# Kernel tuning notes

Measured on AMD Instinct MI355X. Metric: run time of the kernel, lower is better.

## Reference

```python
import jax, jax.numpy as jnp
import numpy as np

N_NODES = 50000
N_EDGES = 800000
D_IN = 128
D_OUT = 128


def setup_inputs() -> dict:
    key = jax.random.key(0)
    k1, k2, k3, k4 = jax.random.split(key, 4)
    feature = jax.random.normal(k1, (N_NODES, D_IN), dtype=jnp.float32)
    relation_indices = jax.random.randint(k2, (2, N_EDGES), 0, N_NODES, dtype=jnp.int64)
    relation_weight = jax.random.uniform(k3, (N_EDGES, 1), dtype=jnp.float32)
    W = jax.random.normal(k4, (2 * D_IN, D_OUT), dtype=jnp.float32) * (1.0 / np.sqrt(2 * D_IN))
    b = jnp.zeros((D_OUT,), dtype=jnp.float32)
    return {"feature": feature, "relation_indices": relation_indices,
            "relation_weight": relation_weight, "W": W, "b": b}


def reference(feature, relation_indices, relation_weight, W, b):
    dst = relation_indices[0]  # segment ids (aggregation target) [E]
    src = relation_indices[1]  # neighbor ids gathered from feature [E]
    # gather neighbor features and apply edge weights (dropout_rate=0 -> identity)
    feat_n = feature[src] * relation_weight  # [E, D_IN]
    # segment mean over destination nodes
    n = feature.shape[0]
    sums = jax.ops.segment_sum(feat_n, dst, num_segments=n)  # [N, D_IN]
    cnts = jax.ops.segment_sum(jnp.ones((feat_n.shape[0],), dtype=feat_n.dtype), dst, num_segments=n)
    neigh_mean = sums / jnp.maximum(cnts, 1.0)[:, None]
    # concat(self, mean_neighbor) -> linear update
    h = jnp.concatenate([feature, neigh_mean], axis=-1)  # [N, 2*D_IN]
    return h @ W + b  # [N, D_OUT]
```

## Files before the change

### kernel.cpp

```cpp
#include <hip/hip_runtime.h>
#include <hip/hip_bf16.h>
#include <stdint.h>

#define N_NODES 50000
#define N_EDGES 800000
#define D 128
#define NB_SCAN 196

typedef __attribute__((ext_vector_type(8))) short bf16x8;
typedef __attribute__((ext_vector_type(4))) float f32x4;
typedef __attribute__((ext_vector_type(2))) short bf16x2;

#define FEATBF_OFF 0
#define MEANBF_OFF 12800000
#define WSW_OFF    25600000
#define HIST_OFF   25665536
#define OFFS_OFF   25865536
#define CURS_OFF   26065552
#define EDGE_OFF   26265552
#define BSUM_OFF   29465552
#define BOFF_OFF   29466576

__device__ inline short f2bf(float x) {
  union { float f; uint32_t u; } v; v.f = x;
  uint32_t r = v.u + 0x7FFFu + ((v.u >> 16) & 1u);
  return (short)(r >> 16);
}
__device__ inline float bf2f(uint32_t bits16) {
  union { uint32_t u; float f; } v; v.u = bits16 << 16;
  return v.f;
}

__global__ __launch_bounds__(256) void k_prep(const float* __restrict__ feat,
                                              const int* __restrict__ idx,
                                              const float* __restrict__ W,
                                              short* __restrict__ featbf,
                                              int* __restrict__ hist,
                                              short* __restrict__ wsw) {
  int b = blockIdx.x;
  if (b < 3125) {
    int i = (b * 256 + threadIdx.x) * 8;
    f32x4 a0 = *(const f32x4*)(feat + i);
    f32x4 a1 = *(const f32x4*)(feat + i + 4);
    bf16x8 o;
    o[0] = f2bf(a0.x); o[1] = f2bf(a0.y); o[2] = f2bf(a0.z); o[3] = f2bf(a0.w);
    o[4] = f2bf(a1.x); o[5] = f2bf(a1.y); o[6] = f2bf(a1.z); o[7] = f2bf(a1.w);
    *(bf16x8*)(featbf + i) = o;
  } else if (b < 6250) {
    int e = (b - 3125) * 256 + threadIdx.x;
    atomicAdd(&hist[idx[e]], 1);
  } else {
    int t = (b - 6250) * 256 + threadIdx.x;
    int kstep = t >> 9;
    int ntile = (t >> 6) & 7;
    int lane  = t & 63;
    int k0  = kstep * 32 + (lane >> 4) * 8;
    int col = ntile * 16 + (lane & 15);
    bf16x8 o;
    #pragma unroll
    for (int j = 0; j < 8; ++j) o[j] = f2bf(W[(k0 + j) * D + col]);
    *(bf16x8*)(wsw + t * 8) = o;
  }
}

__global__ __launch_bounds__(256) void k_scan1(const int* __restrict__ hist,
                                               int* __restrict__ blockSum) {
  __shared__ int red[256];
  int t = threadIdx.x;
  int i = blockIdx.x * 256 + t;
  red[t] = (i < N_NODES) ? hist[i] : 0;
  __syncthreads();
  #pragma unroll
  for (int s = 128; s > 0; s >>= 1) {
    if (t < s) red[t] += red[t + s];
    __syncthreads();
  }
  if (t == 0) blockSum[blockIdx.x] = red[0];
}

__global__ __launch_bounds__(256) void k_scan2(const int* __restrict__ blockSum,
                                               int* __restrict__ blockOff,
                                               int* __restrict__ offs) {
  __shared__ int lds[256];
  int t = threadIdx.x;
  int v = (t < NB_SCAN) ? blockSum[t] : 0;
  lds[t] = v;
  __syncthreads();
  #pragma unroll
  for (int off = 1; off < 256; off <<= 1) {
    int add = (t >= off) ? lds[t - off] : 0;
    __syncthreads();
    lds[t] += add;
    __syncthreads();
  }
  if (t < NB_SCAN) blockOff[t] = lds[t] - v;
  if (t == 255) offs[N_NODES] = lds[255];
}

__global__ __launch_bounds__(256) void k_scan3(const int* __restrict__ hist,
                                               const int* __restrict__ blockOff,
                                               int* __restrict__ offs,
                                               int* __restrict__ cursor) {
  __shared__ int lds[256];
  int t = threadIdx.x;
  int i = blockIdx.x * 256 + t;
  int v = (i < N_NODES) ? hist[i] : 0;
  lds[t] = v;
  __syncthreads();
  #pragma unroll
  for (int off = 1; off < 256; off <<= 1) {
    int add = (t >= off) ? lds[t - off] : 0;
    __syncthreads();
    lds[t] += add;
    __syncthreads();
  }
  int excl = lds[t] - v + blockOff[blockIdx.x];
  if (i < N_NODES) { offs[i] = excl; cursor[i] = excl; }
}

__global__ __launch_bounds__(256) void k_scatter(const int* __restrict__ idx,
                                                 const float* __restrict__ w,
                                                 int* __restrict__ cursor,
                                                 uint32_t* __restrict__ edge) {
  int e = blockIdx.x * 256 + threadIdx.x;
  if (e < N_EDGES) {
    int dst = idx[e];
    int p = atomicAdd(&cursor[dst], 1);
    uint32_t src = (uint32_t)idx[N_EDGES + e];
    uint32_t wb  = (uint32_t)f2bf(w[e]) & 0xFFFFu;
    edge[p] = (src << 16) | wb;
  }
}

__global__ __launch_bounds__(256) void k_agg(const short* __restrict__ featbf,
                                             const int* __restrict__ offs,
                                             const uint32_t* __restrict__ edge,
                                             short* __restrict__ meanbf) {
  int t = blockIdx.x * 256 + threadIdx.x;
  int node = t >> 6;
  int c = t & 63;
  if (node >= N_NODES) return;
  int beg = offs[node], end = offs[node + 1];

  float a0 = 0.f, a1 = 0.f, b0 = 0.f, b1 = 0.f;
  float c0 = 0.f, c1 = 0.f, d0 = 0.f, d1 = 0.f;

  int j = beg;
  for (; j + 3 < end; j += 4) {
    uint32_t e0 = edge[j + 0];
    uint32_t e1 = edge[j + 1];
    uint32_t e2 = edge[j + 2];
    uint32_t e3 = edge[j + 3];
    bf16x2 f0 = *(const bf16x2*)(featbf + (size_t)(e0 >> 16) * D + c * 2);
    bf16x2 f1 = *(const bf16x2*)(featbf + (size_t)(e1 >> 16) * D + c * 2);
    bf16x2 f2 = *(const bf16x2*)(featbf + (size_t)(e2 >> 16) * D + c * 2);
    bf16x2 f3 = *(const bf16x2*)(featbf + (size_t)(e3 >> 16) * D + c * 2);
    float w0 = bf2f(e0 & 0xFFFFu), w1 = bf2f(e1 & 0xFFFFu);
    float w2 = bf2f(e2 & 0xFFFFu), w3 = bf2f(e3 & 0xFFFFu);
    a0 += bf2f((uint16_t)f0[0]) * w0;  a1 += bf2f((uint16_t)f0[1]) * w0;
    b0 += bf2f((uint16_t)f1[0]) * w1;  b1 += bf2f((uint16_t)f1[1]) * w1;
    c0 += bf2f((uint16_t)f2[0]) * w2;  c1 += bf2f((uint16_t)f2[1]) * w2;
    d0 += bf2f((uint16_t)f3[0]) * w3;  d1 += bf2f((uint16_t)f3[1]) * w3;
  }
  for (; j < end; ++j) {
    uint32_t ed = edge[j];
    float wt = bf2f(ed & 0xFFFFu);
    bf16x2 f = *(const bf16x2*)(featbf + (size_t)(ed >> 16) * D + c * 2);
    a0 += bf2f((uint16_t)f[0]) * wt;
    a1 += bf2f((uint16_t)f[1]) * wt;
  }
  float s0 = (a0 + b0) + (c0 + d0);
  float s1 = (a1 + b1) + (c1 + d1);

  float invc = 1.0f / fmaxf((float)(end - beg), 1.0f);
  bf16x2 o;
  o[0] = f2bf(s0 * invc);
  o[1] = f2bf(s1 * invc);
  *(bf16x2*)(meanbf + (size_t)node * D + c * 2) = o;
}

__global__ __launch_bounds__(256) void k_gemm(const short* __restrict__ featbf,
                                              const short* __restrict__ meanbf,
                                              const short* __restrict__ wsw,
                                              const float* __restrict__ bias,
                                              float* __restrict__ out) {
  int wave = threadIdx.x >> 6;
  int lane = threadIdx.x & 63;
  int waveId = blockIdx.x * 4 + wave;
  int R = waveId * 16;
  if (R >= N_NODES) return;

  int row_l = lane & 15;
  int kq    = lane >> 4;
  int myrow = R + row_l;

  f32x4 acc[8];
  #pragma unroll
  for (int nt = 0; nt < 8; ++nt) acc[nt] = (f32x4){0.f, 0.f, 0.f, 0.f};

  #pragma unroll
  for (int kstep = 0; kstep < 8; ++kstep) {
    int kbase = (kstep & 3) * 32 + kq * 8;
    const short* srcrow = (kstep < 4) ? (featbf + (size_t)myrow * D + kbase)
                                      : (meanbf + (size_t)myrow * D + kbase);
    bf16x8 af = *(const bf16x8*)srcrow;
    const bf16x8* wrow = (const bf16x8*)(wsw + ((size_t)kstep * 8 * 64 + lane) * 8);
    #pragma unroll
    for (int nt = 0; nt < 8; ++nt) {
      bf16x8 bf = wrow[nt * 64];
      acc[nt] = __builtin_amdgcn_mfma_f32_16x16x32_bf16(af, bf, acc[nt], 0, 0, 0);
    }
  }

  #pragma unroll
  for (int nt = 0; nt < 8; ++nt) {
    int col = nt * 16 + row_l;
    float bv = bias[col];
    #pragma unroll
    for (int r = 0; r < 4; ++r) {
      int orow = R + kq * 4 + r;
      out[(size_t)orow * D + col] = acc[nt][r] + bv;
    }
  }
}

extern "C" void kernel_launch(void* const* d_in, const int* in_sizes, int n_in,
                              void* d_out, int out_size, void* d_ws, size_t ws_size,
                              hipStream_t stream) {
  const float* feature = (const float*)d_in[0];
  const int*   rel_idx = (const int*)d_in[1];
  const float* rel_w   = (const float*)d_in[2];
  const float* W       = (const float*)d_in[3];
  const float* b       = (const float*)d_in[4];
  float* out = (float*)d_out;

  char* ws = (char*)d_ws;
  short*    featbf = (short*)(ws + FEATBF_OFF);
  short*    meanbf = (short*)(ws + MEANBF_OFF);
  short*    wsw    = (short*)(ws + WSW_OFF);
  int*      hist   = (int*)(ws + HIST_OFF);
  int*      offs   = (int*)(ws + OFFS_OFF);
  int*      curs   = (int*)(ws + CURS_OFF);
  uint32_t* edge   = (uint32_t*)(ws + EDGE_OFF);
  int*      bsum   = (int*)(ws + BSUM_OFF);
  int*      boff   = (int*)(ws + BOFF_OFF);

  hipMemsetAsync(hist, 0, N_NODES * sizeof(int), stream);
  k_prep<<<6266, 256, 0, stream>>>(feature, rel_idx, W, featbf, hist, wsw);
  k_scan1<<<NB_SCAN, 256, 0, stream>>>(hist, bsum);
  k_scan2<<<1, 256, 0, stream>>>(bsum, boff, offs);
  k_scan3<<<NB_SCAN, 256, 0, stream>>>(hist, boff, offs, curs);
  k_scatter<<<(N_EDGES + 255) / 256, 256, 0, stream>>>(rel_idx, rel_w, curs, edge);
  k_agg<<<(N_NODES * 64 + 255) / 256, 256, 0, stream>>>(featbf, offs, edge, meanbf);
  int gemmBlocks = (N_NODES / 16 + 3) / 4;
  k_gemm<<<gemmBlocks, 256, 0, stream>>>(featbf, meanbf, wsw, b, out);
}
```

Baseline: 229.6 us.

## Replace global-atomic edge scatter with two-pass bucketed partition and LDS scatter

The single scatter kernel, which did one global atomic per edge on a per-node cursor, is replaced by two passes. The first bins edges into 256-node buckets split into 16 sub-segments by block index, using far fewer contended counters. The second pass has one block per bucket place the edges into CSR order using LDS atomics. It adds a staging buffer that aliases the mean buffer and assumes a fixed capacity of 512 per segment, which overflows if any bucket sub-segment gets more edges than that (roughly 256 are expected).

```diff
diff --git a/kernel.cpp b/kernel.cpp
--- a/kernel.cpp
+++ b/kernel.cpp
@@ -6,6 +6,8 @@
 #define N_EDGES 800000
 #define D 128
 #define NB_SCAN 196
+#define NSEG 16
+#define SEGCAP 512
 
 typedef __attribute__((ext_vector_type(8))) short bf16x8;
 typedef __attribute__((ext_vector_type(4))) float f32x4;
@@ -13,13 +15,14 @@
 
 #define FEATBF_OFF 0
 #define MEANBF_OFF 12800000
-#define WSW_OFF    25600000
+#define STAGE_OFF  12800000
 #define HIST_OFF   25665536
-#define OFFS_OFF   25865536
-#define CURS_OFF   26065552
-#define EDGE_OFF   26265552
-#define BSUM_OFF   29465552
-#define BOFF_OFF   29466576
+#define CUR2_OFF   25865536
+#define OFFS_OFF   25878080
+#define EDGE_OFF   26078096
+#define BSUM_OFF   29278096
+#define BOFF_OFF   29279120
+#define WSW_OFF    29280144
 
 __device__ inline short f2bf(float x) {
   union { float f; uint32_t u; } v; v.f = x;
@@ -99,8 +102,7 @@
 
 __global__ __launch_bounds__(256) void k_scan3(const int* __restrict__ hist,
                                                const int* __restrict__ blockOff,
-                                               int* __restrict__ offs,
-                                               int* __restrict__ cursor) {
+                                               int* __restrict__ offs) {
   __shared__ int lds[256];
   int t = threadIdx.x;
   int i = blockIdx.x * 256 + t;
@@ -115,20 +117,46 @@
     __syncthreads();
   }
   int excl = lds[t] - v + blockOff[blockIdx.x];
-  if (i < N_NODES) { offs[i] = excl; cursor[i] = excl; }
-}
-
-__global__ __launch_bounds__(256) void k_scatter(const int* __restrict__ idx,
-                                                 const float* __restrict__ w,
-                                                 int* __restrict__ cursor,
-                                                 uint32_t* __restrict__ edge) {
+  if (i < N_NODES) offs[i] = excl;
+}
+
+__global__ __launch_bounds__(256) void k_part(const int* __restrict__ idx,
+                                              const float* __restrict__ w,
+                                              int* __restrict__ cur2,
+                                              uint2* __restrict__ stage) {
   int e = blockIdx.x * 256 + threadIdx.x;
-  if (e < N_EDGES) {
-    int dst = idx[e];
-    int p = atomicAdd(&cursor[dst], 1);
-    uint32_t src = (uint32_t)idx[N_EDGES + e];
-    uint32_t wb  = (uint32_t)f2bf(w[e]) & 0xFFFFu;
-    edge[p] = (src << 16) | wb;
+  int xcls = blockIdx.x & (NSEG - 1);
+  int dst = idx[e];
+  int buk = dst >> 8;
+  int p = atomicAdd(&cur2[buk * NSEG + xcls], 1);
+  uint32_t payload = ((uint32_t)idx[N_EDGES + e] << 16) | ((uint32_t)f2bf(w[e]) & 0xFFFFu);
+  stage[(size_t)(buk * NSEG + xcls) * SEGCAP + p] = make_uint2(payload, (uint32_t)(dst & 255));
+}
+
+__global__ __launch_bounds__(256) void k_scat2(const int* __restrict__ offs,
+                                               const int* __restrict__ cur2,
+                                               const uint2* __restrict__ stage,
+                                               uint32_t* __restrict__ edge) {
+  __shared__ int base[256];
+  __shared__ int cnt[256];
+  __shared__ int slen[NSEG];
+  int buk = blockIdx.x;
+  int t = threadIdx.x;
+  int node = buk * 256 + t;
+  base[t] = (node < N_NODES) ? offs[node] : 0;
+  cnt[t] = 0;
+  if (t < NSEG) slen[t] = cur2[buk * NSEG + t];
+  __syncthreads();
+  #pragma unroll 1
+  for (int s = 0; s < NSEG; ++s) {
+    int len = slen[s];
+    const uint2* seg = stage + (size_t)(buk * NSEG + s) * SEGCAP;
+    for (int i = t; i < len; i += 256) {
+      uint2 it = seg[i];
+      int dl = (int)it.y;
+      int p = atomicAdd(&cnt[dl], 1);
+      edge[base[dl] + p] = it.x;
+    }
   }
 }
 
@@ -237,20 +265,22 @@
   char* ws = (char*)d_ws;
   short*    featbf = (short*)(ws + FEATBF_OFF);
   short*    meanbf = (short*)(ws + MEANBF_OFF);
-  short*    wsw    = (short*)(ws + WSW_OFF);
+  uint2*    stage  = (uint2*)(ws + STAGE_OFF);
   int*      hist   = (int*)(ws + HIST_OFF);
+  int*      cur2   = (int*)(ws + CUR2_OFF);
   int*      offs   = (int*)(ws + OFFS_OFF);
-  int*      curs   = (int*)(ws + CURS_OFF);
   uint32_t* edge   = (uint32_t*)(ws + EDGE_OFF);
   int*      bsum   = (int*)(ws + BSUM_OFF);
   int*      boff   = (int*)(ws + BOFF_OFF);
-
-  hipMemsetAsync(hist, 0, N_NODES * sizeof(int), stream);
+  short*    wsw    = (short*)(ws + WSW_OFF);
+
+  hipMemsetAsync(hist, 0, (CUR2_OFF - HIST_OFF) + NB_SCAN * NSEG * sizeof(int), stream);
   k_prep<<<6266, 256, 0, stream>>>(feature, rel_idx, W, featbf, hist, wsw);
   k_scan1<<<NB_SCAN, 256, 0, stream>>>(hist, bsum);
   k_scan2<<<1, 256, 0, stream>>>(bsum, boff, offs);
-  k_scan3<<<NB_SCAN, 256, 0, stream>>>(hist, boff, offs, curs);
-  k_scatter<<<(N_EDGES + 255) / 256, 256, 0, stream>>>(rel_idx, rel_w, curs, edge);
+  k_scan3<<<NB_SCAN, 256, 0, stream>>>(hist, boff, offs);
+  k_part<<<3125, 256, 0, stream>>>(rel_idx, rel_w, cur2, stage);
+  k_scat2<<<NB_SCAN, 256, 0, stream>>>(offs, cur2, stage, edge);
   k_agg<<<(N_NODES * 64 + 255) / 256, 256, 0, stream>>>(featbf, offs, edge, meanbf);
   int gemmBlocks = (N_NODES / 16 + 3) / 4;
   k_gemm<<<gemmBlocks, 256, 0, stream>>>(featbf, meanbf, wsw, b, out);
```

Result: slower. 274.1 us (+19.4%).
